# Kernel tuning notes

Measured on AMD Instinct MI355X. Metric: run time of the kernel, lower is better.

## Reference

```python
import jax, jax.numpy as jnp
import numpy as np

EPS = 1e-5

def _bn(h, gamma, beta):
    # BatchNorm1d in training mode: per-channel stats over the batch dim (L=1)
    m = jnp.mean(h, axis=0)
    v = jnp.var(h, axis=0)  # biased variance, as torch uses for normalization
    return gamma * (h - m) * jax.lax.rsqrt(v + EPS) + beta

def setup_inputs() -> dict:
    key = jax.random.key(0)
    ks = jax.random.split(key, 8)
    vocab, emb = 8192, 512
    inter = (vocab + emb) // 2  # 4352
    N = 8192
    x_t = jax.random.randint(ks[0], (N,), 0, vocab, dtype=jnp.int64)
    W1 = jax.random.normal(ks[1], (inter, vocab), dtype=jnp.float32) * 0.02
    b1 = jax.random.normal(ks[2], (inter,), dtype=jnp.float32) * 0.02
    g1 = jnp.ones((inter,), dtype=jnp.float32)
    beta1 = jnp.zeros((inter,), dtype=jnp.float32)
    W2 = jax.random.normal(ks[3], (emb, inter), dtype=jnp.float32) * 0.02
    b2 = jax.random.normal(ks[4], (emb,), dtype=jnp.float32) * 0.02
    g2 = jnp.ones((emb,), dtype=jnp.float32)
    beta2 = jnp.zeros((emb,), dtype=jnp.float32)
    return {"x_t": x_t, "W1": W1, "b1": b1, "g1": g1, "beta1": beta1,
            "W2": W2, "b2": b2, "g2": g2, "beta2": beta2}

def reference(x_t, W1, b1, g1, beta1, W2, b2, g2, beta2):
    # one_hot(x_t) @ Conv1d(k=1) weight == gather of W1 columns (same math, no dense one-hot)
    h1 = W1.T[x_t] + b1                      # [N, inter]
    h1 = jax.nn.gelu(_bn(h1, g1, beta1), approximate=False)
    h2 = h1 @ W2.T + b2                      # [N, emb]
    out = jax.nn.gelu(_bn(h2, g2, beta2), approximate=False)
    return out
```

## Files before the change

### kernel.cpp

```cpp
#include <hip/hip_runtime.h>
#include <hip/hip_bf16.h>
#include <math.h>

typedef __attribute__((ext_vector_type(8))) short short8;
typedef __attribute__((ext_vector_type(4))) float f32x4;

#define VOCAB 8192
#define NSAMP 8192
#define INTER 4352
#define EMB   512

#define OFF_CNT    0
#define OFF_A1     32768
#define OFF_M1     50176
#define OFF_A2     67584
#define OFF_M2     69632
#define OFF_PS1B   71680
#define OFF_PS2B   1120256
#define OFF_W2B    2168832
#define OFF_HACT   6625280
#define OFF_HPART  77928448
#define PART_BYTES 16777216ULL

__device__ __forceinline__ float gelu_exact(float x) {
    return 0.5f * x * (1.0f + erff(x * 0.70710678118654752f));
}
__device__ __forceinline__ unsigned short f2bf(float x) {
    __hip_bfloat16 b = __float2bfloat16(x);
    return *reinterpret_cast<unsigned short*>(&b);
}
__device__ __forceinline__ void async16(const unsigned short* g, unsigned short* l) {
    __builtin_amdgcn_global_load_lds(
        (const __attribute__((address_space(1))) void*)g,
        (__attribute__((address_space(3))) void*)l, 16, 0, 0);
}

__global__ void k_zero_cnt(int* cnt) {
    cnt[blockIdx.x * 256 + threadIdx.x] = 0;
}
__global__ void k_hist(const int* __restrict__ xt, int* __restrict__ cnt) {
    int n = blockIdx.x * 256 + threadIdx.x;
    atomicAdd(&cnt[xt[n]], 1);
}

__global__ __launch_bounds__(256) void k_stats1(const float* __restrict__ W1,
                                                const int* __restrict__ cnt,
                                                const float* __restrict__ g1,
                                                float* __restrict__ a1,
                                                float* __restrict__ m1) {
    const int t = threadIdx.x, lane = t & 63, w = t >> 6;
    const int row = blockIdx.x * 4 + w;
    const float* wr = W1 + (size_t)row * VOCAB;
    float s1 = 0.f, s2 = 0.f;
    #pragma unroll 8
    for (int it = 0; it < 32; ++it) {
        int v = it * 256 + lane * 4;
        float4 x = *(const float4*)(wr + v);
        int4 c = *(const int4*)(cnt + v);
        float cx = (float)c.x, cy = (float)c.y, cz = (float)c.z, cw = (float)c.w;
        s1 += cx * x.x + cy * x.y + cz * x.z + cw * x.w;
        s2 += cx * x.x * x.x + cy * x.y * x.y + cz * x.z * x.z + cw * x.w * x.w;
    }
    #pragma unroll
    for (int d = 1; d < 64; d <<= 1) {
        s1 += __shfl_xor(s1, d);
        s2 += __shfl_xor(s2, d);
    }
    if (lane == 0) {
        float m = s1 * (1.f / NSAMP);
        float var = s2 * (1.f / NSAMP) - m * m;
        a1[row] = g1[row] * rsqrtf(var + 1e-5f);
        m1[row] = m;
    }
}

__global__ __launch_bounds__(256) void k_build(const float* __restrict__ W1,
                                               const float* __restrict__ a1,
                                               const float* __restrict__ m1,
                                               const float* __restrict__ beta1,
                                               unsigned short* __restrict__ Hact) {
    const int i0 = blockIdx.x * 64;
    const int v0 = blockIdx.y * 256;
    const int t = threadIdx.x;
    const int c0 = (t & 15) * 4;
    const int vg = (t >> 4) * 4;
    float4 av = *(const float4*)(a1 + i0 + c0);
    float4 mv = *(const float4*)(m1 + i0 + c0);
    float4 bv = *(const float4*)(beta1 + i0 + c0);
    const float* ap = (const float*)&av;
    const float* mp = (const float*)&mv;
    const float* bp = (const float*)&bv;
    #pragma unroll
    for (int vi = 0; vi < 4; ++vi) {
        int vb = v0 + vi * 64 + vg;
        float wf[4][4];
        #pragma unroll
        for (int j = 0; j < 4; ++j)
            *(float4*)&wf[j][0] = *(const float4*)(W1 + (size_t)(i0 + c0 + j) * VOCAB + vb);
        #pragma unroll
        for (int k = 0; k < 4; ++k) {
            ushort4 o;
            o.x = f2bf(gelu_exact(ap[0] * (wf[0][k] - mp[0]) + bp[0]));
            o.y = f2bf(gelu_exact(ap[1] * (wf[1][k] - mp[1]) + bp[1]));
            o.z = f2bf(gelu_exact(ap[2] * (wf[2][k] - mp[2]) + bp[2]));
            o.w = f2bf(gelu_exact(ap[3] * (wf[3][k] - mp[3]) + bp[3]));
            *(ushort4*)&Hact[(size_t)(vb + k) * INTER + i0 + c0] = o;
        }
    }
}

__global__ void k_w2bf(const float* __restrict__ W2, unsigned short* __restrict__ W2b) {
    int idx = (blockIdx.x * 256 + threadIdx.x) * 4;
    float4 w = *(const float4*)(W2 + idx);
    ushort4 u;
    u.x = f2bf(w.x); u.y = f2bf(w.y); u.z = f2bf(w.z); u.w = f2bf(w.w);
    *(ushort4*)(W2b + idx) = u;
}

__global__ __launch_bounds__(512) void k_gemm(const unsigned short* __restrict__ A,
                                              const unsigned short* __restrict__ B,
                                              float* __restrict__ Cp, int kPer) {
    __shared__ __align__(16) unsigned short sA[128 * 64];
    __shared__ __align__(16) unsigned short sB[512 * 64];
    const int m0 = blockIdx.x * 128;
    const int kbeg = blockIdx.z * kPer;
    const int kend = kbeg + kPer;
    float* C = Cp + (size_t)blockIdx.z * NSAMP * EMB;
    const int t = threadIdx.x;
    const int lane = t & 63;
    const int wave = t >> 6;
    const int wr = wave >> 2, wc = wave & 3;
    const int mq = lane & 15, kq = lane >> 4;
    const int srow = lane >> 3;
    const int sgrp = lane & 7;
    const int scol = (sgrp ^ srow) * 8;
    const int swz = mq & 7;
    f32x4 acc[4][8];
    #pragma unroll
    for (int r = 0; r < 4; ++r)
        #pragma unroll
        for (int c = 0; c < 8; ++c) acc[r][c] = (f32x4){0.f, 0.f, 0.f, 0.f};
    for (int k0 = kbeg; k0 < kend; k0 += 64) {
        #pragma unroll
        for (int p = 0; p < 2; ++p) {
            int r0 = wave * 16 + p * 8;
            async16(A + (size_t)(m0 + r0 + srow) * INTER + k0 + scol, &sA[r0 * 64]);
        }
        #pragma unroll
        for (int p = 0; p < 8; ++p) {
            int r0 = wave * 64 + p * 8;
            async16(B + (size_t)(r0 + srow) * INTER + k0 + scol, &sB[r0 * 64]);
        }
        __syncthreads();
        #pragma unroll
        for (int kk = 0; kk < 64; kk += 32) {
            const int gbase = kq + (kk >> 3);
            short8 af[4], bf[8];
            #pragma unroll
            for (int r = 0; r < 4; ++r)
                af[r] = *(const short8*)&sA[(wr * 64 + r * 16 + mq) * 64 + ((gbase ^ swz) * 8)];
            #pragma unroll
            for (int c = 0; c < 8; ++c)
                bf[c] = *(const short8*)&sB[(wc * 128 + c * 16 + mq) * 64 + ((gbase ^ swz) * 8)];
            #pragma unroll
            for (int r = 0; r < 4; ++r)
                #pragma unroll
                for (int c = 0; c < 8; ++c)
                    acc[r][c] = __builtin_amdgcn_mfma_f32_16x16x32_bf16(af[r], bf[c], acc[r][c], 0, 0, 0);
        }
        __syncthreads();
    }
    #pragma unroll
    for (int r = 0; r < 4; ++r) {
        #pragma unroll
        for (int c = 0; c < 8; ++c) {
            int col = wc * 128 + c * 16 + mq;
            int rowb = m0 + wr * 64 + r * 16 + kq * 4;
            #pragma unroll
            for (int j = 0; j < 4; ++j)
                C[(size_t)(rowb + j) * EMB + col] = acc[r][c][j];
        }
    }
}

__global__ __launch_bounds__(256) void k_reduce(const float* hpart,
                                                const int* __restrict__ cnt,
                                                float* h2,
                                                float* __restrict__ ps1,
                                                float* __restrict__ ps2, int S) {
    __shared__ float4 b1[128], b2[128];
    const int v0 = blockIdx.x * 16;
    const int t = threadIdx.x;
    const int half = t >> 7;
    const int c4 = (t & 127) * 4;
    float4 acc1 = {0.f, 0.f, 0.f, 0.f}, acc2 = {0.f, 0.f, 0.f, 0.f};
    #pragma unroll
    for (int rp = 0; rp < 8; ++rp) {
        int r = v0 + rp * 2 + half;
        int cw_i = cnt[r];
        if (cw_i > 0) {
            size_t off = (size_t)r * EMB + c4;
            float4 h = *(const float4*)(hpart + off);
            for (int s = 1; s < S; ++s) {
                float4 hs = *(const float4*)(hpart + (size_t)s * NSAMP * EMB + off);
                h.x += hs.x; h.y += hs.y; h.z += hs.z; h.w += hs.w;
            }
            *(float4*)(h2 + off) = h;
            float w = (float)cw_i;
            acc1.x += w * h.x; acc1.y += w * h.y; acc1.z += w * h.z; acc1.w += w * h.w;
            acc2.x += w * h.x * h.x; acc2.y += w * h.y * h.y;
            acc2.z += w * h.z * h.z; acc2.w += w * h.w * h.w;
        }
    }
    if (half == 1) { b1[t & 127] = acc1; b2[t & 127] = acc2; }
    __syncthreads();
    if (half == 0) {
        float4 o1 = b1[t & 127], o2 = b2[t & 127];
        o1.x += acc1.x; o1.y += acc1.y; o1.z += acc1.z; o1.w += acc1.w;
        o2.x += acc2.x; o2.y += acc2.y; o2.z += acc2.z; o2.w += acc2.w;
        ps1[(size_t)(c4 + 0) * 512 + blockIdx.x] = o1.x;
        ps1[(size_t)(c4 + 1) * 512 + blockIdx.x] = o1.y;
        ps1[(size_t)(c4 + 2) * 512 + blockIdx.x] = o1.z;
        ps1[(size_t)(c4 + 3) * 512 + blockIdx.x] = o1.w;
        ps2[(size_t)(c4 + 0) * 512 + blockIdx.x] = o2.x;
        ps2[(size_t)(c4 + 1) * 512 + blockIdx.x] = o2.y;
        ps2[(size_t)(c4 + 2) * 512 + blockIdx.x] = o2.z;
        ps2[(size_t)(c4 + 3) * 512 + blockIdx.x] = o2.w;
    }
}

__global__ __launch_bounds__(256) void k_stats2f(const float* __restrict__ ps1,
                                                 const float* __restrict__ ps2,
                                                 const float* __restrict__ g2,
                                                 float* __restrict__ a2,
                                                 float* __restrict__ m2) {
    const int lane = threadIdx.x & 63;
    const int e = blockIdx.x * 4 + (threadIdx.x >> 6);
    float s1 = 0.f, s2 = 0.f;
    #pragma unroll
    for (int k = 0; k < 8; ++k) {
        s1 += ps1[(size_t)e * 512 + k * 64 + lane];
        s2 += ps2[(size_t)e * 512 + k * 64 + lane];
    }
    #pragma unroll
    for (int d = 1; d < 64; d <<= 1) {
        s1 += __shfl_xor(s1, d);
        s2 += __shfl_xor(s2, d);
    }
    if (lane == 0) {
        float m = s1 * (1.f / NSAMP);
        float var = s2 * (1.f / NSAMP) - m * m;
        a2[e] = g2[e] * rsqrtf(var + 1e-5f);
        m2[e] = m;
    }
}

__global__ __launch_bounds__(256) void k_final(const float* __restrict__ h2,
                                               const int* __restrict__ xt,
                                               const float* __restrict__ a2,
                                               const float* __restrict__ m2,
                                               const float* __restrict__ beta2,
                                               float* __restrict__ out) {
    const int t = threadIdx.x;
    const int n = blockIdx.x * 2 + (t >> 7);
    const int e = (t & 127) * 4;
    const int v = xt[n];
    float4 h = *(const float4*)(h2 + (size_t)v * EMB + e);
    float4 a = *(const float4*)(a2 + e);
    float4 m = *(const float4*)(m2 + e);
    float4 b = *(const float4*)(beta2 + e);
    float4 o;
    o.x = gelu_exact(a.x * (h.x - m.x) + b.x);
    o.y = gelu_exact(a.y * (h.y - m.y) + b.y);
    o.z = gelu_exact(a.z * (h.z - m.z) + b.z);
    o.w = gelu_exact(a.w * (h.w - m.w) + b.w);
    *(float4*)(out + (size_t)n * EMB + e) = o;
}

extern "C" void kernel_launch(void* const* d_in, const int* in_sizes, int n_in,
                              void* d_out, int out_size, void* d_ws, size_t ws_size,
                              hipStream_t stream) {
    const int* xt      = (const int*)d_in[0];
    const float* W1    = (const float*)d_in[1];
    const float* g1    = (const float*)d_in[3];
    const float* beta1 = (const float*)d_in[4];
    const float* W2    = (const float*)d_in[5];
    const float* g2    = (const float*)d_in[7];
    const float* beta2 = (const float*)d_in[8];
    float* out = (float*)d_out;

    char* ws = (char*)d_ws;
    int*   cnt  = (int*)  (ws + OFF_CNT);
    float* a1   = (float*)(ws + OFF_A1);
    float* m1   = (float*)(ws + OFF_M1);
    float* a2   = (float*)(ws + OFF_A2);
    float* m2   = (float*)(ws + OFF_M2);
    float* ps1b = (float*)(ws + OFF_PS1B);
    float* ps2b = (float*)(ws + OFF_PS2B);
    unsigned short* W2b  = (unsigned short*)(ws + OFF_W2B);
    unsigned short* Hact = (unsigned short*)(ws + OFF_HACT);
    float* hpart = (float*)(ws + OFF_HPART);
    float* h2 = hpart;

    int S = 1;
    if (ws_size >= OFF_HPART + 4 * PART_BYTES) S = 4;
    else if (ws_size >= OFF_HPART + 2 * PART_BYTES) S = 2;

    k_zero_cnt<<<32, 256, 0, stream>>>(cnt);
    k_hist<<<32, 256, 0, stream>>>(xt, cnt);
    k_stats1<<<1088, 256, 0, stream>>>(W1, cnt, g1, a1, m1);
    k_build<<<dim3(68, 32), 256, 0, stream>>>(W1, a1, m1, beta1, Hact);
    k_w2bf<<<2176, 256, 0, stream>>>(W2, W2b);
    k_gemm<<<dim3(64, 1, S), 512, 0, stream>>>(Hact, W2b, hpart, INTER / S);
    k_reduce<<<512, 256, 0, stream>>>(hpart, cnt, h2, ps1b, ps2b, S);
    k_stats2f<<<128, 256, 0, stream>>>(ps1b, ps2b, g2, a2, m2);
    k_final<<<4096, 256, 0, stream>>>(h2, xt, a2, m2, beta2, out);
}
```

Measured before the change: 356.4 us.

## Fuse BN2 stats into GEMM epilogue, drop split-K, add double-buffered tiles

The GEMM grid changes from a split-K 64×S layout with 128×512 tiles to 256 blocks of 128×128 tiles with full K. The K loop now uses double-buffered LDS staging so the next tile's loads overlap the current MFMA work. The count-weighted sum and sum-of-squares for the second BatchNorm move into the GEMM epilogue, which removes the separate reduce kernel and the partial-sum round trip through memory. The tradeoff is smaller tiles with less B reuse per block, and occupancy now depends on the 256-block grid.

```diff
diff --git a/kernel.cpp b/kernel.cpp
--- a/kernel.cpp
+++ b/kernel.cpp
@@ -19,8 +19,7 @@
 #define OFF_PS2B   1120256
 #define OFF_W2B    2168832
 #define OFF_HACT   6625280
-#define OFF_HPART  77928448
-#define PART_BYTES 16777216ULL
+#define OFF_H2     77928448
 
 __device__ __forceinline__ float gelu_exact(float x) {
     return 0.5f * x * (1.0f + erff(x * 0.70710678118654752f));
@@ -119,13 +118,17 @@
 
 __global__ __launch_bounds__(512) void k_gemm(const unsigned short* __restrict__ A,
                                               const unsigned short* __restrict__ B,
-                                              float* __restrict__ Cp, int kPer) {
-    __shared__ __align__(16) unsigned short sA[128 * 64];
-    __shared__ __align__(16) unsigned short sB[512 * 64];
-    const int m0 = blockIdx.x * 128;
-    const int kbeg = blockIdx.z * kPer;
-    const int kend = kbeg + kPer;
-    float* C = Cp + (size_t)blockIdx.z * NSAMP * EMB;
+                                              const int* __restrict__ cnt,
+                                              float* __restrict__ h2,
+                                              float* __restrict__ ps1,
+                                              float* __restrict__ ps2) {
+    __shared__ __align__(16) unsigned short sA[2][128 * 64];
+    __shared__ __align__(16) unsigned short sB[2][128 * 64];
+    const int bid = blockIdx.x;
+    const int mblk = bid >> 2;
+    const int nblk = bid & 3;
+    const int m0 = mblk * 128;
+    const int n0 = nblk * 128;
     const int t = threadIdx.x;
     const int lane = t & 63;
     const int wave = t >> 6;
@@ -135,97 +138,83 @@
     const int sgrp = lane & 7;
     const int scol = (sgrp ^ srow) * 8;
     const int swz = mq & 7;
-    f32x4 acc[4][8];
+
+    const unsigned short* Ab = A + (size_t)(m0 + wave * 16 + srow) * INTER + scol;
+    const unsigned short* Bb = B + (size_t)(n0 + wave * 16 + srow) * INTER + scol;
+
+    f32x4 acc[4][2];
     #pragma unroll
     for (int r = 0; r < 4; ++r)
         #pragma unroll
-        for (int c = 0; c < 8; ++c) acc[r][c] = (f32x4){0.f, 0.f, 0.f, 0.f};
-    for (int k0 = kbeg; k0 < kend; k0 += 64) {
-        #pragma unroll
-        for (int p = 0; p < 2; ++p) {
-            int r0 = wave * 16 + p * 8;
-            async16(A + (size_t)(m0 + r0 + srow) * INTER + k0 + scol, &sA[r0 * 64]);
-        }
-        #pragma unroll
-        for (int p = 0; p < 8; ++p) {
-            int r0 = wave * 64 + p * 8;
-            async16(B + (size_t)(r0 + srow) * INTER + k0 + scol, &sB[r0 * 64]);
-        }
-        __syncthreads();
+        for (int c = 0; c < 2; ++c) acc[r][c] = (f32x4){0.f, 0.f, 0.f, 0.f};
+
+    auto stage = [&](int buf, int k0) {
+        async16(Ab + k0,                         &sA[buf][(wave * 16) * 64]);
+        async16(Ab + (size_t)8 * INTER + k0,     &sA[buf][(wave * 16 + 8) * 64]);
+        async16(Bb + k0,                         &sB[buf][(wave * 16) * 64]);
+        async16(Bb + (size_t)8 * INTER + k0,     &sB[buf][(wave * 16 + 8) * 64]);
+    };
+    auto compute = [&](int buf) {
         #pragma unroll
         for (int kk = 0; kk < 64; kk += 32) {
             const int gbase = kq + (kk >> 3);
-            short8 af[4], bf[8];
+            short8 af[4], bfr[2];
             #pragma unroll
             for (int r = 0; r < 4; ++r)
-                af[r] = *(const short8*)&sA[(wr * 64 + r * 16 + mq) * 64 + ((gbase ^ swz) * 8)];
+                af[r] = *(const short8*)&sA[buf][(wr * 64 + r * 16 + mq) * 64 + ((gbase ^ swz) * 8)];
             #pragma unroll
-            for (int c = 0; c < 8; ++c)
-                bf[c] = *(const short8*)&sB[(wc * 128 + c * 16 + mq) * 64 + ((gbase ^ swz) * 8)];
+            for (int c = 0; c < 2; ++c)
+                bfr[c] = *(const short8*)&sB[buf][(wc * 32 + c * 16 + mq) * 64 + ((gbase ^ swz) * 8)];
             #pragma unroll
             for (int r = 0; r < 4; ++r)
                 #pragma unroll
-                for (int c = 0; c < 8; ++c)
-                    acc[r][c] = __builtin_amdgcn_mfma_f32_16x16x32_bf16(af[r], bf[c], acc[r][c], 0, 0, 0);
-        }
+                for (int c = 0; c < 2; ++c)
+                    acc[r][c] = __builtin_amdgcn_mfma_f32_16x16x32_bf16(af[r], bfr[c], acc[r][c], 0, 0, 0);
+        }
+    };
+
+    stage(0, 0);
+    __syncthreads();
+    for (int ti = 0; ti < 67; ++ti) {
+        stage((ti + 1) & 1, (ti + 1) * 64);
+        compute(ti & 1);
         __syncthreads();
     }
+    compute(1);
+
+    float s1[2] = {0.f, 0.f}, s2[2] = {0.f, 0.f};
     #pragma unroll
     for (int r = 0; r < 4; ++r) {
-        #pragma unroll
-        for (int c = 0; c < 8; ++c) {
-            int col = wc * 128 + c * 16 + mq;
-            int rowb = m0 + wr * 64 + r * 16 + kq * 4;
-            #pragma unroll
-            for (int j = 0; j < 4; ++j)
-                C[(size_t)(rowb + j) * EMB + col] = acc[r][c][j];
-        }
-    }
-}
-
-__global__ __launch_bounds__(256) void k_reduce(const float* hpart,
-                                                const int* __restrict__ cnt,
-                                                float* h2,
-                                                float* __restrict__ ps1,
-                                                float* __restrict__ ps2, int S) {
-    __shared__ float4 b1[128], b2[128];
-    const int v0 = blockIdx.x * 16;
-    const int t = threadIdx.x;
-    const int half = t >> 7;
-    const int c4 = (t & 127) * 4;
-    float4 acc1 = {0.f, 0.f, 0.f, 0.f}, acc2 = {0.f, 0.f, 0.f, 0.f};
-    #pragma unroll
-    for (int rp = 0; rp < 8; ++rp) {
-        int r = v0 + rp * 2 + half;
-        int cw_i = cnt[r];
-        if (cw_i > 0) {
-            size_t off = (size_t)r * EMB + c4;
-            float4 h = *(const float4*)(hpart + off);
-            for (int s = 1; s < S; ++s) {
-                float4 hs = *(const float4*)(hpart + (size_t)s * NSAMP * EMB + off);
-                h.x += hs.x; h.y += hs.y; h.z += hs.z; h.w += hs.w;
-            }
-            *(float4*)(h2 + off) = h;
-            float w = (float)cw_i;
-            acc1.x += w * h.x; acc1.y += w * h.y; acc1.z += w * h.z; acc1.w += w * h.w;
-            acc2.x += w * h.x * h.x; acc2.y += w * h.y * h.y;
-            acc2.z += w * h.z * h.z; acc2.w += w * h.w * h.w;
-        }
-    }
-    if (half == 1) { b1[t & 127] = acc1; b2[t & 127] = acc2; }
-    __syncthreads();
-    if (half == 0) {
-        float4 o1 = b1[t & 127], o2 = b2[t & 127];
-        o1.x += acc1.x; o1.y += acc1.y; o1.z += acc1.z; o1.w += acc1.w;
-        o2.x += acc2.x; o2.y += acc2.y; o2.z += acc2.z; o2.w += acc2.w;
-        ps1[(size_t)(c4 + 0) * 512 + blockIdx.x] = o1.x;
-        ps1[(size_t)(c4 + 1) * 512 + blockIdx.x] = o1.y;
-        ps1[(size_t)(c4 + 2) * 512 + blockIdx.x] = o1.z;
-        ps1[(size_t)(c4 + 3) * 512 + blockIdx.x] = o1.w;
-        ps2[(size_t)(c4 + 0) * 512 + blockIdx.x] = o2.x;
-        ps2[(size_t)(c4 + 1) * 512 + blockIdx.x] = o2.y;
-        ps2[(size_t)(c4 + 2) * 512 + blockIdx.x] = o2.z;
-        ps2[(size_t)(c4 + 3) * 512 + blockIdx.x] = o2.w;
+        const int rowb = m0 + wr * 64 + r * 16 + kq * 4;
+        int4 cw = *(const int4*)(cnt + rowb);
+        float w0 = (float)cw.x, w1 = (float)cw.y, w2 = (float)cw.z, w3 = (float)cw.w;
+        #pragma unroll
+        for (int c = 0; c < 2; ++c) {
+            const int col = n0 + wc * 32 + c * 16 + mq;
+            float v0 = acc[r][c][0], v1 = acc[r][c][1], v2 = acc[r][c][2], v3 = acc[r][c][3];
+            h2[(size_t)(rowb + 0) * EMB + col] = v0;
+            h2[(size_t)(rowb + 1) * EMB + col] = v1;
+            h2[(size_t)(rowb + 2) * EMB + col] = v2;
+            h2[(size_t)(rowb + 3) * EMB + col] = v3;
+            s1[c] += w0 * v0 + w1 * v1 + w2 * v2 + w3 * v3;
+            s2[c] += w0 * v0 * v0 + w1 * v1 * v1 + w2 * v2 * v2 + w3 * v3 * v3;
+        }
+    }
+    #pragma unroll
+    for (int c = 0; c < 2; ++c) {
+        s1[c] += __shfl_xor(s1[c], 16);
+        s2[c] += __shfl_xor(s2[c], 16);
+        s1[c] += __shfl_xor(s1[c], 32);
+        s2[c] += __shfl_xor(s2[c], 32);
+    }
+    if (lane < 16) {
+        const int slot = mblk * 2 + wr;
+        #pragma unroll
+        for (int c = 0; c < 2; ++c) {
+            const int col = n0 + wc * 32 + c * 16 + mq;
+            ps1[(size_t)col * 128 + slot] = s1[c];
+            ps2[(size_t)col * 128 + slot] = s2[c];
+        }
     }
 }
 
@@ -236,12 +225,8 @@
                                                  float* __restrict__ m2) {
     const int lane = threadIdx.x & 63;
     const int e = blockIdx.x * 4 + (threadIdx.x >> 6);
-    float s1 = 0.f, s2 = 0.f;
-    #pragma unroll
-    for (int k = 0; k < 8; ++k) {
-        s1 += ps1[(size_t)e * 512 + k * 64 + lane];
-        s2 += ps2[(size_t)e * 512 + k * 64 + lane];
-    }
+    float s1 = ps1[(size_t)e * 128 + lane] + ps1[(size_t)e * 128 + 64 + lane];
+    float s2 = ps2[(size_t)e * 128 + lane] + ps2[(size_t)e * 128 + 64 + lane];
     #pragma unroll
     for (int d = 1; d < 64; d <<= 1) {
         s1 += __shfl_xor(s1, d);
@@ -299,20 +284,14 @@
     float* ps2b = (float*)(ws + OFF_PS2B);
     unsigned short* W2b  = (unsigned short*)(ws + OFF_W2B);
     unsigned short* Hact = (unsigned short*)(ws + OFF_HACT);
-    float* hpart = (float*)(ws + OFF_HPART);
-    float* h2 = hpart;
-
-    int S = 1;
-    if (ws_size >= OFF_HPART + 4 * PART_BYTES) S = 4;
-    else if (ws_size >= OFF_HPART + 2 * PART_BYTES) S = 2;
+    float* h2   = (float*)(ws + OFF_H2);
 
     k_zero_cnt<<<32, 256, 0, stream>>>(cnt);
     k_hist<<<32, 256, 0, stream>>>(xt, cnt);
     k_stats1<<<1088, 256, 0, stream>>>(W1, cnt, g1, a1, m1);
     k_build<<<dim3(68, 32), 256, 0, stream>>>(W1, a1, m1, beta1, Hact);
     k_w2bf<<<2176, 256, 0, stream>>>(W2, W2b);
-    k_gemm<<<dim3(64, 1, S), 512, 0, stream>>>(Hact, W2b, hpart, INTER / S);
-    k_reduce<<<512, 256, 0, stream>>>(hpart, cnt, h2, ps1b, ps2b, S);
+    k_gemm<<<256, 512, 0, stream>>>(Hact, W2b, cnt, h2, ps1b, ps2b);
     k_stats2f<<<128, 256, 0, stream>>>(ps1b, ps2b, g2, a2, m2);
     k_final<<<4096, 256, 0, stream>>>(h2, xt, a2, m2, beta2, out);
 }
```

Measured after the change: 344.1 us. -3.4%, faster.

## Retile GEMM to 128x128 double-buffered blocks and fuse small prep kernels

Applied to the files above, without the earlier changes.

The GEMM now uses 128x128 output tiles over a flat grid of 256*S blocks, where each block previously covered the full 512-wide N dimension. It double-buffers the LDS stages so the next tile's async loads overlap MFMA work, and raises wave priority around the MFMAs. Split-K is capped at 2. Separately, the histogram becomes a single block using a shared-memory histogram with no zeroing kernel, and the W2 bf16 conversion is folded into the build kernel's grid, which removes launches. Smaller tiles give more blocks to spread across CUs but lower data reuse per block.

```diff
diff --git a/kernel.cpp b/kernel.cpp
--- a/kernel.cpp
+++ b/kernel.cpp
@@ -19,7 +19,7 @@
 #define OFF_PS2B   1120256
 #define OFF_W2B    2168832
 #define OFF_HACT   6625280
-#define OFF_HPART  77928448
+#define OFF_H2     77928448
 #define PART_BYTES 16777216ULL
 
 __device__ __forceinline__ float gelu_exact(float x) {
@@ -35,12 +35,23 @@
         (__attribute__((address_space(3))) void*)l, 16, 0, 0);
 }
 
-__global__ void k_zero_cnt(int* cnt) {
-    cnt[blockIdx.x * 256 + threadIdx.x] = 0;
-}
-__global__ void k_hist(const int* __restrict__ xt, int* __restrict__ cnt) {
-    int n = blockIdx.x * 256 + threadIdx.x;
-    atomicAdd(&cnt[xt[n]], 1);
+__global__ __launch_bounds__(1024) void k_hist1b(const int* __restrict__ xt,
+                                                 int* __restrict__ cnt) {
+    __shared__ int h[VOCAB];
+    const int t = threadIdx.x;
+    #pragma unroll
+    for (int i = 0; i < 8; ++i) h[t + i * 1024] = 0;
+    __syncthreads();
+    const int4* x4 = (const int4*)xt;
+    int4 a = x4[t], b = x4[t + 1024];
+    atomicAdd(&h[a.x], 1); atomicAdd(&h[a.y], 1);
+    atomicAdd(&h[a.z], 1); atomicAdd(&h[a.w], 1);
+    atomicAdd(&h[b.x], 1); atomicAdd(&h[b.y], 1);
+    atomicAdd(&h[b.z], 1); atomicAdd(&h[b.w], 1);
+    __syncthreads();
+    #pragma unroll
+    for (int i = 0; i < 2; ++i)
+        ((int4*)cnt)[t + i * 1024] = ((const int4*)h)[t + i * 1024];
 }
 
 __global__ __launch_bounds__(256) void k_stats1(const float* __restrict__ W1,
@@ -74,14 +85,25 @@
     }
 }
 
-__global__ __launch_bounds__(256) void k_build(const float* __restrict__ W1,
-                                               const float* __restrict__ a1,
-                                               const float* __restrict__ m1,
-                                               const float* __restrict__ beta1,
-                                               unsigned short* __restrict__ Hact) {
-    const int i0 = blockIdx.x * 64;
-    const int v0 = blockIdx.y * 256;
-    const int t = threadIdx.x;
+__global__ __launch_bounds__(256) void k_buildw2(const float* __restrict__ W1,
+                                                 const float* __restrict__ a1,
+                                                 const float* __restrict__ m1,
+                                                 const float* __restrict__ beta1,
+                                                 unsigned short* __restrict__ Hact,
+                                                 const float* __restrict__ W2,
+                                                 unsigned short* __restrict__ W2b) {
+    const int bx = blockIdx.x;
+    const int t = threadIdx.x;
+    if (bx >= 2176) {
+        int idx = ((bx - 2176) * 256 + t) * 4;
+        float4 w = *(const float4*)(W2 + idx);
+        ushort4 u;
+        u.x = f2bf(w.x); u.y = f2bf(w.y); u.z = f2bf(w.z); u.w = f2bf(w.w);
+        *(ushort4*)(W2b + idx) = u;
+        return;
+    }
+    const int i0 = (bx % 68) * 64;
+    const int v0 = (bx / 68) * 256;
     const int c0 = (t & 15) * 4;
     const int vg = (t >> 4) * 4;
     float4 av = *(const float4*)(a1 + i0 + c0);
@@ -109,23 +131,20 @@
     }
 }
 
-__global__ void k_w2bf(const float* __restrict__ W2, unsigned short* __restrict__ W2b) {
-    int idx = (blockIdx.x * 256 + threadIdx.x) * 4;
-    float4 w = *(const float4*)(W2 + idx);
-    ushort4 u;
-    u.x = f2bf(w.x); u.y = f2bf(w.y); u.z = f2bf(w.z); u.w = f2bf(w.w);
-    *(ushort4*)(W2b + idx) = u;
-}
-
 __global__ __launch_bounds__(512) void k_gemm(const unsigned short* __restrict__ A,
                                               const unsigned short* __restrict__ B,
-                                              float* __restrict__ Cp, int kPer) {
-    __shared__ __align__(16) unsigned short sA[128 * 64];
-    __shared__ __align__(16) unsigned short sB[512 * 64];
-    const int m0 = blockIdx.x * 128;
-    const int kbeg = blockIdx.z * kPer;
-    const int kend = kbeg + kPer;
-    float* C = Cp + (size_t)blockIdx.z * NSAMP * EMB;
+                                              float* __restrict__ hpart, int kPer) {
+    __shared__ __align__(16) unsigned short sA[2][128 * 64];
+    __shared__ __align__(16) unsigned short sB[2][128 * 64];
+    const int bid = blockIdx.x;
+    const int mblk = bid & 63;
+    const int nblk = (bid >> 6) & 3;
+    const int ks   = bid >> 8;
+    const int m0 = mblk * 128;
+    const int n0 = nblk * 128;
+    const int kbeg = ks * kPer;
+    const int nsteps = kPer >> 6;
+    float* C = hpart + (size_t)ks * NSAMP * EMB;
     const int t = threadIdx.x;
     const int lane = t & 63;
     const int wave = t >> 6;
@@ -135,47 +154,60 @@
     const int sgrp = lane & 7;
     const int scol = (sgrp ^ srow) * 8;
     const int swz = mq & 7;
-    f32x4 acc[4][8];
+
+    const unsigned short* Ab = A + (size_t)(m0 + wave * 16 + srow) * INTER + kbeg + scol;
+    const unsigned short* Bb = B + (size_t)(n0 + wave * 16 + srow) * INTER + kbeg + scol;
+
+    f32x4 acc[4][2];
     #pragma unroll
     for (int r = 0; r < 4; ++r)
         #pragma unroll
-        for (int c = 0; c < 8; ++c) acc[r][c] = (f32x4){0.f, 0.f, 0.f, 0.f};
-    for (int k0 = kbeg; k0 < kend; k0 += 64) {
-        #pragma unroll
-        for (int p = 0; p < 2; ++p) {
-            int r0 = wave * 16 + p * 8;
-            async16(A + (size_t)(m0 + r0 + srow) * INTER + k0 + scol, &sA[r0 * 64]);
-        }
-        #pragma unroll
-        for (int p = 0; p < 8; ++p) {
-            int r0 = wave * 64 + p * 8;
-            async16(B + (size_t)(r0 + srow) * INTER + k0 + scol, &sB[r0 * 64]);
-        }
-        __syncthreads();
+        for (int c = 0; c < 2; ++c) acc[r][c] = (f32x4){0.f, 0.f, 0.f, 0.f};
+
+    auto stage = [&](int buf, int tile) {
+        const int k0 = tile * 64;
+        async16(Ab + k0,                     &sA[buf][(wave * 16) * 64]);
+        async16(Ab + (size_t)8 * INTER + k0, &sA[buf][(wave * 16 + 8) * 64]);
+        async16(Bb + k0,                     &sB[buf][(wave * 16) * 64]);
+        async16(Bb + (size_t)8 * INTER + k0, &sB[buf][(wave * 16 + 8) * 64]);
+    };
+    auto compute = [&](int buf) {
         #pragma unroll
         for (int kk = 0; kk < 64; kk += 32) {
             const int gbase = kq + (kk >> 3);
-            short8 af[4], bf[8];
+            short8 af[4], bfr[2];
             #pragma unroll
             for (int r = 0; r < 4; ++r)
-                af[r] = *(const short8*)&sA[(wr * 64 + r * 16 + mq) * 64 + ((gbase ^ swz) * 8)];
+                af[r] = *(const short8*)&sA[buf][(wr * 64 + r * 16 + mq) * 64 + ((gbase ^ swz) * 8)];
             #pragma unroll
-            for (int c = 0; c < 8; ++c)
-                bf[c] = *(const short8*)&sB[(wc * 128 + c * 16 + mq) * 64 + ((gbase ^ swz) * 8)];
+            for (int c = 0; c < 2; ++c)
+                bfr[c] = *(const short8*)&sB[buf][(wc * 32 + c * 16 + mq) * 64 + ((gbase ^ swz) * 8)];
+            __builtin_amdgcn_s_setprio(1);
             #pragma unroll
             for (int r = 0; r < 4; ++r)
                 #pragma unroll
-                for (int c = 0; c < 8; ++c)
-                    acc[r][c] = __builtin_amdgcn_mfma_f32_16x16x32_bf16(af[r], bf[c], acc[r][c], 0, 0, 0);
+                for (int c = 0; c < 2; ++c)
+                    acc[r][c] = __builtin_amdgcn_mfma_f32_16x16x32_bf16(af[r], bfr[c], acc[r][c], 0, 0, 0);
+            __builtin_amdgcn_s_setprio(0);
         }
+    };
+
+    stage(0, 0);
+    __syncthreads();
+    #pragma unroll 1
+    for (int ti = 0; ti < nsteps - 1; ++ti) {
+        stage((ti + 1) & 1, ti + 1);
+        compute(ti & 1);
         __syncthreads();
     }
+    compute((nsteps - 1) & 1);
+
     #pragma unroll
     for (int r = 0; r < 4; ++r) {
-        #pragma unroll
-        for (int c = 0; c < 8; ++c) {
-            int col = wc * 128 + c * 16 + mq;
-            int rowb = m0 + wr * 64 + r * 16 + kq * 4;
+        const int rowb = m0 + wr * 64 + r * 16 + kq * 4;
+        #pragma unroll
+        for (int c = 0; c < 2; ++c) {
+            const int col = n0 + wc * 32 + c * 16 + mq;
             #pragma unroll
             for (int j = 0; j < 4; ++j)
                 C[(size_t)(rowb + j) * EMB + col] = acc[r][c][j];
@@ -299,19 +331,15 @@
     float* ps2b = (float*)(ws + OFF_PS2B);
     unsigned short* W2b  = (unsigned short*)(ws + OFF_W2B);
     unsigned short* Hact = (unsigned short*)(ws + OFF_HACT);
-    float* hpart = (float*)(ws + OFF_HPART);
+    float* hpart = (float*)(ws + OFF_H2);
     float* h2 = hpart;
 
-    int S = 1;
-    if (ws_size >= OFF_HPART + 4 * PART_BYTES) S = 4;
-    else if (ws_size >= OFF_HPART + 2 * PART_BYTES) S = 2;
-
-    k_zero_cnt<<<32, 256, 0, stream>>>(cnt);
-    k_hist<<<32, 256, 0, stream>>>(xt, cnt);
+    const int S = (ws_size >= OFF_H2 + 2 * PART_BYTES) ? 2 : 1;
+
+    k_hist1b<<<1, 1024, 0, stream>>>(xt, cnt);
     k_stats1<<<1088, 256, 0, stream>>>(W1, cnt, g1, a1, m1);
-    k_build<<<dim3(68, 32), 256, 0, stream>>>(W1, a1, m1, beta1, Hact);
-    k_w2bf<<<2176, 256, 0, stream>>>(W2, W2b);
-    k_gemm<<<dim3(64, 1, S), 512, 0, stream>>>(Hact, W2b, hpart, INTER / S);
+    k_buildw2<<<4352, 256, 0, stream>>>(W1, a1, m1, beta1, Hact, W2, W2b);
+    k_gemm<<<256 * S, 512, 0, stream>>>(Hact, W2b, hpart, INTER / S);
     k_reduce<<<512, 256, 0, stream>>>(hpart, cnt, h2, ps1b, ps2b, S);
     k_stats2f<<<128, 256, 0, stream>>>(ps1b, ps2b, g2, a2, m2);
     k_final<<<4096, 256, 0, stream>>>(h2, xt, a2, m2, beta2, out);
```

Result: faster. 322.9 us (-9.4%).
